# Optimization experiments

Hardware: AMD Instinct MI355X
Metric: run time of the kernel (lower is better)

## Reference

```python
import jax, jax.numpy as jnp
import numpy as np

B, S, D, H = 4, 2048, 1024, 16
DK = D // H
SCALE = float(np.sqrt(DK))
NEG_INF = jnp.float32(-1e30)


def setup_inputs() -> dict:
    key = jax.random.key(0)
    ks = jax.random.split(key, 12)
    std = 1.0 / np.sqrt(D)
    def lin(k):
        kw, kb = jax.random.split(k)
        W = jax.random.uniform(kw, (D, D), jnp.float32, -std, std)
        b = jax.random.uniform(kb, (D,), jnp.float32, -std, std)
        return W, b
    Wq, bq = lin(ks[0]); Wk, bk = lin(ks[1]); Wv, bv = lin(ks[2]); Wo, bo = lin(ks[3])
    query = jax.random.normal(ks[4], (B, S, D), jnp.float32)
    key_t = jax.random.normal(ks[5], (B, S, D), jnp.float32)
    value = jax.random.normal(ks[6], (B, S, D), jnp.float32)
    # causal mask, broadcastable to [B,H,S,S]; positions where mask==0 are blocked
    mask = jnp.tril(jnp.ones((S, S), dtype=bool))[None, None]
    return {"query": query, "key": key_t, "value": value,
            "Wq": Wq, "bq": bq, "Wk": Wk, "bk": bk, "Wv": Wv, "bv": bv,
            "Wo": Wo, "bo": bo, "mask": mask}


def reference(query, key, value, Wq, bq, Wk, bk, Wv, bv, Wo, bo, mask):
    # projections: x @ W.T + b (torch nn.Linear convention)
    q = (query @ Wq.T + bq).reshape(B, S, H, DK).transpose(0, 2, 1, 3)  # [B,H,S,DK]
    k = (key @ Wk.T + bk).reshape(B, S, H, DK).transpose(0, 2, 1, 3)
    v = (value @ Wv.T + bv).reshape(B, S, H, DK).transpose(0, 2, 1, 3)
    scores = jnp.einsum('bhqd,bhkd->bhqk', q, k) / SCALE  # [B,H,S,S]
    scores = jnp.where(mask, scores, NEG_INF)
    attn = jax.nn.softmax(scores, axis=-1)
    # dropout is identity in eval / p used at train only; omitted (p treated as 0)
    context = jnp.einsum('bhqk,bhkd->bhqd', attn, v)  # [B,H,S,DK]
    context = context.transpose(0, 2, 1, 3).reshape(B, S, D)
    return context @ Wo.T + bo
```

## Files before the change

### kernel.cpp

```cpp
#include <hip/hip_runtime.h>
#include <hip/hip_bf16.h>
#include <cstdint>
#include <cstddef>


namespace {

constexpr int B  = 4;
constexpr int S  = 2048;
constexpr int D  = 1024;
constexpr int H  = 16;
constexpr int DK = 64;
constexpr int M  = B * S;
constexpr float LOG2E    = 1.44269504088896f;
constexpr float QSCALE   = 0.125f * LOG2E;
constexpr float NEG_BIG  = -1e30f;
constexpr float DEFER_THR = 8.0f;

using bf16 = __hip_bfloat16;

typedef __attribute__((ext_vector_type(8))) __bf16 bf16x8;
typedef __attribute__((ext_vector_type(4))) float  f32x4;

__device__ __forceinline__ uint16_t f2bfu(float x) {
  uint32_t a = __builtin_bit_cast(uint32_t, x);
  return (uint16_t)((a + 0x7FFFu + ((a >> 16) & 1u)) >> 16);
}
__device__ __forceinline__ uint32_t pk2(float x, float y) {
  return (uint32_t)f2bfu(x) | ((uint32_t)f2bfu(y) << 16);
}
__device__ __forceinline__ float ex2(float x) {
  float r; asm("v_exp_f32 %0, %1" : "=v"(r) : "v"(x)); return r;
}

__device__ __forceinline__ void ldst16(const uint4* g, uint4* l) {
  __builtin_amdgcn_global_load_lds(
      (const __attribute__((address_space(1))) void*)g,
      (__attribute__((address_space(3))) void*)l, 16, 0, 0);
}

__global__ __launch_bounds__(256)
void cvt_f2b(const float* __restrict__ src, bf16* __restrict__ dst, int n8)
{
  const int i = blockIdx.x * 256 + threadIdx.x;
  if (i >= n8) return;
  const float4 a = ((const float4*)src)[2 * i];
  const float4 b = ((const float4*)src)[2 * i + 1];
  uint4 r;
  r.x = pk2(a.x, a.y); r.y = pk2(a.z, a.w);
  r.z = pk2(b.x, b.y); r.w = pk2(b.z, b.w);
  ((uint4*)dst)[i] = r;
}

template <int MODE>
__global__ __launch_bounds__(256)
void gemm128(const bf16* __restrict__ A, const bf16* __restrict__ Wb,
             const float* __restrict__ bias, void* __restrict__ out,
             int N, int K, float scale)
{
  __shared__ uint4 AsU[2][1024];
  __shared__ uint4 BsU[2][1024];

  const int tid  = threadIdx.x;
  const int w    = tid >> 6;
  const int lane = tid & 63;
  const int lm   = lane & 15;
  const int quad = lane >> 4;
  const int wm   = (w >> 1) * 64;
  const int wn   = (w & 1) * 64;

  const int row0 = blockIdx.y * 128, col0 = blockIdx.x * 128;
  const int g8 = K >> 3;

  const uint4* Ag = (const uint4*)A + (size_t)row0 * g8;
  const uint4* Bg = (const uint4*)Wb + (size_t)col0 * g8;

  f32x4 acc[4][4] = {};
  const int KT = K / 64;

#pragma unroll
  for (int i = 0; i < 4; ++i) {
    const int chunk = i * 256 + w * 64 + lane;
    const int r = chunk >> 3, c = chunk & 7;
    ldst16(&Ag[(size_t)r * g8 + c], &AsU[0][i * 256 + w * 64]);
    ldst16(&Bg[(size_t)r * g8 + c], &BsU[0][i * 256 + w * 64]);
  }

  int cur = 0;
  for (int kt = 0; kt < KT; ++kt) {
    __syncthreads();
    if (kt + 1 < KT) {
#pragma unroll
      for (int i = 0; i < 4; ++i) {
        const int chunk = i * 256 + w * 64 + lane;
        const int r = chunk >> 3, c = chunk & 7;
        ldst16(&Ag[(size_t)r * g8 + (kt + 1) * 8 + c], &AsU[cur ^ 1][i * 256 + w * 64]);
        ldst16(&Bg[(size_t)r * g8 + (kt + 1) * 8 + c], &BsU[cur ^ 1][i * 256 + w * 64]);
      }
    }
#pragma unroll
    for (int kk = 0; kk < 2; ++kk) {
      bf16x8 af[4], bfr[4];
#pragma unroll
      for (int tm = 0; tm < 4; ++tm)
        af[tm] = __builtin_bit_cast(bf16x8, AsU[cur][(wm + tm * 16 + lm) * 8 + kk * 4 + quad]);
#pragma unroll
      for (int tn = 0; tn < 4; ++tn)
        bfr[tn] = __builtin_bit_cast(bf16x8, BsU[cur][(wn + tn * 16 + lm) * 8 + kk * 4 + quad]);
#pragma unroll
      for (int tm = 0; tm < 4; ++tm)
#pragma unroll
        for (int tn = 0; tn < 4; ++tn)
          acc[tm][tn] = __builtin_amdgcn_mfma_f32_16x16x32_bf16(af[tm], bfr[tn], acc[tm][tn], 0, 0, 0);
    }
    cur ^= 1;
  }

#pragma unroll
  for (int tm = 0; tm < 4; ++tm) {
#pragma unroll
    for (int tn = 0; tn < 4; ++tn) {
      const int col = col0 + wn + tn * 16 + lm;
      const float bv = bias[col];
      if (MODE == 2) {
        float vv[4];
#pragma unroll
        for (int r = 0; r < 4; ++r) vv[r] = (acc[tm][tn][r] + bv) * scale;
        const int s0 = row0 + wm + tm * 16 + quad * 4;
        const int b_ = s0 >> 11, ss = s0 & (S - 1);
        const int h_ = col >> 6, dk = col & (DK - 1);
        uint2 st; st.x = pk2(vv[0], vv[1]); st.y = pk2(vv[2], vv[3]);
        *(uint2*)((bf16*)out + (((size_t)b_ * H + h_) * DK + dk) * S + ss) = st;
      } else {
#pragma unroll
        for (int r = 0; r < 4; ++r) {
          const int row = row0 + wm + tm * 16 + quad * 4 + r;
          const float v = (acc[tm][tn][r] + bv) * scale;
          if (MODE == 0) {
            ((float*)out)[(size_t)row * N + col] = v;
          } else {
            const int b_ = row >> 11, s_ = row & (S - 1);
            const int h_ = col >> 6,  dk = col & (DK - 1);
            ((bf16*)out)[(((size_t)b_ * H + h_) * S + s_) * DK + dk] =
                __builtin_bit_cast(bf16, f2bfu(v));
          }
        }
      }
    }
  }
}

__global__ __launch_bounds__(512)
void flash_mfma(const bf16* __restrict__ Q, const bf16* __restrict__ K,
                const bf16* __restrict__ Vt, bf16* __restrict__ ctx)
{
  __shared__ uint4 KsU[2][512];
  __shared__ uint4 VtU[2][512];
  __shared__ uint16_t PsAll[128 * 72];

  const int tid  = threadIdx.x;
  const int w    = tid >> 6;
  const int lane = tid & 63;
  const int lm   = lane & 15;
  const int quad = lane >> 4;
  const int bh   = blockIdx.x;
  const int pr   = blockIdx.y;
  const size_t base = (size_t)bh * S * DK;

  const uint4* Kg0 = (const uint4*)(K + base);
  const uint4* Vg0 = (const uint4*)(Vt + (size_t)bh * DK * S);

  const int rr   = w * 8 + (lane >> 3);
  const int csw  = (lane & 7) ^ (lane >> 3);
  const int swz0 = quad ^ (lm & 7);

  uint16_t* const Pw = PsAll + (w * 16) * 72;
  const int b_ = bh >> 4, h_ = bh & (H - 1);

  for (int pass = 0; pass < 2; ++pass) {
    const int qi = pass ? (15 - pr) : pr;
    const int q0 = qi * 128;
    const int qbase = q0 + w * 16;

    bf16x8 qf0, qf1;
    {
      const bf16* qrow = Q + base + (size_t)(qbase + lm) * DK;
      qf0 = __builtin_bit_cast(bf16x8, *(const uint4*)(qrow + quad * 8));
      qf1 = __builtin_bit_cast(bf16x8, *(const uint4*)(qrow + 32 + quad * 8));
    }

    f32x4 o[4] = {};
    float m_i[4], l_i[4];
#pragma unroll
    for (int r = 0; r < 4; ++r) { m_i[r] = NEG_BIG; l_i[r] = 0.f; }

    const int nt = 2 * qi + 2;

    ldst16(&Kg0[(size_t)rr * 8 + csw],        &KsU[0][w * 64]);
    ldst16(&Vg0[(size_t)rr * (S / 8) + csw],  &VtU[0][w * 64]);

    int cur = 0;
    for (int t = 0; t < nt; ++t) {
      __syncthreads();
      if (t + 1 < nt) {
        const int k1 = (t + 1) * 64;
        ldst16(&Kg0[(size_t)(k1 + rr) * 8 + csw],         &KsU[cur ^ 1][w * 64]);
        ldst16(&Vg0[(size_t)rr * (S / 8) + k1 / 8 + csw], &VtU[cur ^ 1][w * 64]);
      }
      const int k0 = t * 64;
      if (k0 <= qbase + 15) {
        const uint4* Ks = KsU[cur];
        const uint4* Vs = VtU[cur];

        f32x4 sc[4];
        __builtin_amdgcn_s_setprio(1);
#pragma unroll
        for (int tn = 0; tn < 4; ++tn) {
          const int row = tn * 16 + lm;
          bf16x8 kb0 = __builtin_bit_cast(bf16x8, Ks[row * 8 + swz0]);
          bf16x8 kb1 = __builtin_bit_cast(bf16x8, Ks[row * 8 + (swz0 ^ 4)]);
          sc[tn] = __builtin_amdgcn_mfma_f32_16x16x32_bf16(
                       qf0, kb0, f32x4{0.f, 0.f, 0.f, 0.f}, 0, 0, 0);
          sc[tn] = __builtin_amdgcn_mfma_f32_16x16x32_bf16(qf1, kb1, sc[tn], 0, 0, 0);
        }
        __builtin_amdgcn_s_setprio(0);

        if (k0 + 63 > qbase) {
          const int qg = qbase + quad * 4;
#pragma unroll
          for (int tn = 0; tn < 4; ++tn) {
            const int kg_ = k0 + tn * 16 + lm;
#pragma unroll
            for (int r = 0; r < 4; ++r)
              if (kg_ > qg + r) sc[tn][r] = NEG_BIG;
          }
        }

        float mr[4];
        bool need = false;
#pragma unroll
        for (int r = 0; r < 4; ++r) {
          float m4 = fmaxf(fmaxf(sc[0][r], sc[1][r]), fmaxf(sc[2][r], sc[3][r]));
#pragma unroll
          for (int off = 8; off; off >>= 1) m4 = fmaxf(m4, __shfl_xor(m4, off));
          mr[r] = m4;
          need = need || (m4 > m_i[r] + DEFER_THR);
        }
        if (__any(need)) {
#pragma unroll
          for (int r = 0; r < 4; ++r) {
            const float mn = fmaxf(m_i[r], mr[r]);
            const float al = ex2(m_i[r] - mn);
            l_i[r] *= al;
#pragma unroll
            for (int tn = 0; tn < 4; ++tn) o[tn][r] *= al;
            m_i[r] = mn;
          }
        }
#pragma unroll
        for (int r = 0; r < 4; ++r) {
          float ls = 0.f;
#pragma unroll
          for (int tn = 0; tn < 4; ++tn) {
            const float p = ex2(sc[tn][r] - m_i[r]);
            ls += p;
            Pw[(quad * 4 + r) * 72 + tn * 16 + lm] = f2bfu(p);
          }
          l_i[r] += ls;
        }

        bf16x8 ap0, ap1;
        {
          const uint16_t* prp = Pw + lm * 72 + quad * 8;
          ap0 = __builtin_bit_cast(bf16x8, *(const uint4*)prp);
          ap1 = __builtin_bit_cast(bf16x8, *(const uint4*)(prp + 32));
        }
        __builtin_amdgcn_s_setprio(1);
#pragma unroll
        for (int tn = 0; tn < 4; ++tn) {
          const int row = tn * 16 + lm;
          bf16x8 vb0 = __builtin_bit_cast(bf16x8, Vs[row * 8 + swz0]);
          bf16x8 vb1 = __builtin_bit_cast(bf16x8, Vs[row * 8 + (swz0 ^ 4)]);
          o[tn] = __builtin_amdgcn_mfma_f32_16x16x32_bf16(ap0, vb0, o[tn], 0, 0, 0);
          o[tn] = __builtin_amdgcn_mfma_f32_16x16x32_bf16(ap1, vb1, o[tn], 0, 0, 0);
        }
        __builtin_amdgcn_s_setprio(0);
      }
      cur ^= 1;
    }

    __syncthreads();
#pragma unroll
    for (int r = 0; r < 4; ++r) {
      float lr = l_i[r];
#pragma unroll
      for (int off = 8; off; off >>= 1) lr += __shfl_xor(lr, off);
      const float inv = 1.f / lr;
#pragma unroll
      for (int tn = 0; tn < 4; ++tn)
        Pw[(quad * 4 + r) * 72 + tn * 16 + lm] = f2bfu(o[tn][r] * inv);
    }
    __syncthreads();

#pragma unroll
    for (int i = 0; i < 2; ++i) {
      const int idx = tid + i * 512;
      const int row = idx >> 3, c = idx & 7;
      const uint4 v = *(const uint4*)(PsAll + row * 72 + c * 8);
      *(uint4*)(ctx + ((((size_t)b_ * S + q0 + row) * H + h_) << 6) + c * 8) = v;
    }
  }
}

}

extern "C" void kernel_launch(void* const* d_in, const int* in_sizes, int n_in,
                              void* d_out, int out_size, void* d_ws, size_t ws_size,
                              hipStream_t stream)
{
  const float* query = (const float*)d_in[0];
  const float* key_  = (const float*)d_in[1];
  const float* value = (const float*)d_in[2];
  const float* Wq    = (const float*)d_in[3];
  const float* bq    = (const float*)d_in[4];
  const float* Wk    = (const float*)d_in[5];
  const float* bk    = (const float*)d_in[6];
  const float* Wv    = (const float*)d_in[7];
  const float* bv    = (const float*)d_in[8];
  const float* Wo    = (const float*)d_in[9];
  const float* bo    = (const float*)d_in[10];

  const size_t qkv = (size_t)B * H * S * DK;
  bf16* slot0 = (bf16*)d_ws;
  bf16* slot1 = slot0 + qkv;
  bf16* slot2 = slot1 + qkv;
  bf16* slot3 = slot2 + qkv;
  bf16* inbf  = (bf16*)d_out;

  const int n8in = (int)(qkv / 8);
  const int n8w  = (D * D) / 8;
  const dim3 cvtIn(n8in / 256), cvtW(n8w / 256);
  const dim3 gproj(D / 128, M / 128);
  const dim3 gattn(B * H, 8);

  cvt_f2b<<<cvtIn, 256, 0, stream>>>(query, inbf, n8in);
  cvt_f2b<<<cvtW,  256, 0, stream>>>(Wq, slot3, n8w);
  gemm128<1><<<gproj, 256, 0, stream>>>(inbf, slot3, bq, slot0, D, D, QSCALE);
  cvt_f2b<<<cvtIn, 256, 0, stream>>>(key_, inbf, n8in);
  cvt_f2b<<<cvtW,  256, 0, stream>>>(Wk, slot3, n8w);
  gemm128<1><<<gproj, 256, 0, stream>>>(inbf, slot3, bk, slot1, D, D, 1.0f);
  cvt_f2b<<<cvtIn, 256, 0, stream>>>(value, inbf, n8in);
  cvt_f2b<<<cvtW,  256, 0, stream>>>(Wv, slot3, n8w);
  gemm128<2><<<gproj, 256, 0, stream>>>(inbf, slot3, bv, slot2, D, D, 1.0f);
  flash_mfma<<<gattn, 512, 0, stream>>>(slot0, slot1, slot2, slot3);
  cvt_f2b<<<cvtW, 256, 0, stream>>>(Wo, slot0, n8w);
  gemm128<0><<<gproj, 256, 0, stream>>>(slot3, slot0, bo, d_out, D, D, 1.0f);
}
```

Baseline: 384.1 us.

## Keep softmax P in registers via transposed QK MFMA and batch conversions

```diff
diff --git a/kernel.cpp b/kernel.cpp
--- a/kernel.cpp
+++ b/kernel.cpp
@@ -12,9 +12,9 @@
 constexpr int H  = 16;
 constexpr int DK = 64;
 constexpr int M  = B * S;
-constexpr float LOG2E    = 1.44269504088896f;
-constexpr float QSCALE   = 0.125f * LOG2E;
-constexpr float NEG_BIG  = -1e30f;
+constexpr float LOG2E     = 1.44269504088896f;
+constexpr float QSCALE    = 0.125f * LOG2E;
+constexpr float NEG_BIG   = -1e30f;
 constexpr float DEFER_THR = 8.0f;
 
 using bf16 = __hip_bfloat16;
@@ -31,6 +31,14 @@
 }
 __device__ __forceinline__ float ex2(float x) {
   float r; asm("v_exp_f32 %0, %1" : "=v"(r) : "v"(x)); return r;
+}
+__device__ __forceinline__ uint32_t cvtpk(float lo, float hi) {
+  uint32_t r;
+  asm("v_cvt_pk_bf16_f32 %0, %1, %2" : "=v"(r) : "v"(lo), "v"(hi));
+  return r;
+}
+__device__ __forceinline__ float hmax4(f32x4 v) {
+  return fmaxf(fmaxf(v[0], v[1]), fmaxf(v[2], v[3]));
 }
 
 __device__ __forceinline__ void ldst16(const uint4* g, uint4* l) {
@@ -40,15 +48,20 @@
 }
 
 __global__ __launch_bounds__(256)
-void cvt_f2b(const float* __restrict__ src, bf16* __restrict__ dst, int n8)
+void cvt3(const float* __restrict__ a, const float* __restrict__ b,
+          const float* __restrict__ c, bf16* __restrict__ x,
+          bf16* __restrict__ y, bf16* __restrict__ z_, int n8)
 {
+  const int zz = blockIdx.y;
+  const float* src = (zz == 0) ? a : (zz == 1) ? b : c;
+  bf16*        dst = (zz == 0) ? x : (zz == 1) ? y : z_;
   const int i = blockIdx.x * 256 + threadIdx.x;
   if (i >= n8) return;
-  const float4 a = ((const float4*)src)[2 * i];
-  const float4 b = ((const float4*)src)[2 * i + 1];
+  const float4 p = ((const float4*)src)[2 * i];
+  const float4 q = ((const float4*)src)[2 * i + 1];
   uint4 r;
-  r.x = pk2(a.x, a.y); r.y = pk2(a.z, a.w);
-  r.z = pk2(b.x, b.y); r.w = pk2(b.z, b.w);
+  r.x = pk2(p.x, p.y); r.y = pk2(p.z, p.w);
+  r.z = pk2(q.x, q.y); r.w = pk2(q.z, q.w);
   ((uint4*)dst)[i] = r;
 }
 
@@ -156,7 +169,7 @@
 {
   __shared__ uint4 KsU[2][512];
   __shared__ uint4 VtU[2][512];
-  __shared__ uint16_t PsAll[128 * 72];
+  __shared__ uint16_t Os[128 * 72];
 
   const int tid  = threadIdx.x;
   const int w    = tid >> 6;
@@ -170,11 +183,12 @@
   const uint4* Kg0 = (const uint4*)(K + base);
   const uint4* Vg0 = (const uint4*)(Vt + (size_t)bh * DK * S);
 
-  const int rr   = w * 8 + (lane >> 3);
-  const int csw  = (lane & 7) ^ (lane >> 3);
-  const int swz0 = quad ^ (lm & 7);
-
-  uint16_t* const Pw = PsAll + (w * 16) * 72;
+  const int rr  = w * 8 + (lane >> 3);
+  const int csw = (lane & 7) ^ (lane >> 3) ^ ((w & 1) << 2);
+  const int fv  = (lm & 7) ^ (((lm >> 3) & 1) << 2);
+  const int r0  = ((lm >> 2) << 3) | (lm & 3);
+
+  uint16_t* const Ow = Os + (w * 16) * 72;
   const int b_ = bh >> 4, h_ = bh & (H - 1);
 
   for (int pass = 0; pass < 2; ++pass) {
@@ -190,14 +204,12 @@
     }
 
     f32x4 o[4] = {};
-    float m_i[4], l_i[4];
-#pragma unroll
-    for (int r = 0; r < 4; ++r) { m_i[r] = NEG_BIG; l_i[r] = 0.f; }
+    float m_i = NEG_BIG, l_i = 0.f;
 
     const int nt = 2 * qi + 2;
 
-    ldst16(&Kg0[(size_t)rr * 8 + csw],        &KsU[0][w * 64]);
-    ldst16(&Vg0[(size_t)rr * (S / 8) + csw],  &VtU[0][w * 64]);
+    ldst16(&Kg0[(size_t)rr * 8 + csw],       &KsU[0][w * 64]);
+    ldst16(&Vg0[(size_t)rr * (S / 8) + csw], &VtU[0][w * 64]);
 
     int cur = 0;
     for (int t = 0; t < nt; ++t) {
@@ -216,71 +228,71 @@
         __builtin_amdgcn_s_setprio(1);
 #pragma unroll
         for (int tn = 0; tn < 4; ++tn) {
-          const int row = tn * 16 + lm;
-          bf16x8 kb0 = __builtin_bit_cast(bf16x8, Ks[row * 8 + swz0]);
-          bf16x8 kb1 = __builtin_bit_cast(bf16x8, Ks[row * 8 + (swz0 ^ 4)]);
+          const int row = r0 + ((tn & 1) << 2) + ((tn >> 1) << 5);
+          const int fr  = (row & 7) ^ (((row >> 3) & 1) << 2);
+          const int cb  = quad ^ fr;
+          bf16x8 kb0 = __builtin_bit_cast(bf16x8, Ks[row * 8 + cb]);
+          bf16x8 kb1 = __builtin_bit_cast(bf16x8, Ks[row * 8 + (cb ^ 4)]);
           sc[tn] = __builtin_amdgcn_mfma_f32_16x16x32_bf16(
-                       qf0, kb0, f32x4{0.f, 0.f, 0.f, 0.f}, 0, 0, 0);
-          sc[tn] = __builtin_amdgcn_mfma_f32_16x16x32_bf16(qf1, kb1, sc[tn], 0, 0, 0);
+                       kb0, qf0, f32x4{0.f, 0.f, 0.f, 0.f}, 0, 0, 0);
+          sc[tn] = __builtin_amdgcn_mfma_f32_16x16x32_bf16(kb1, qf1, sc[tn], 0, 0, 0);
         }
         __builtin_amdgcn_s_setprio(0);
 
         if (k0 + 63 > qbase) {
-          const int qg = qbase + quad * 4;
+          const int qg = qbase + lm;
 #pragma unroll
           for (int tn = 0; tn < 4; ++tn) {
-            const int kg_ = k0 + tn * 16 + lm;
+            const int kb_ = k0 + ((tn >> 1) << 5) + (quad << 3) + ((tn & 1) << 2);
 #pragma unroll
             for (int r = 0; r < 4; ++r)
-              if (kg_ > qg + r) sc[tn][r] = NEG_BIG;
+              if (kb_ + r > qg) sc[tn][r] = NEG_BIG;
           }
         }
 
-        float mr[4];
-        bool need = false;
-#pragma unroll
-        for (int r = 0; r < 4; ++r) {
-          float m4 = fmaxf(fmaxf(sc[0][r], sc[1][r]), fmaxf(sc[2][r], sc[3][r]));
-#pragma unroll
-          for (int off = 8; off; off >>= 1) m4 = fmaxf(m4, __shfl_xor(m4, off));
-          mr[r] = m4;
-          need = need || (m4 > m_i[r] + DEFER_THR);
-        }
-        if (__any(need)) {
-#pragma unroll
-          for (int r = 0; r < 4; ++r) {
-            const float mn = fmaxf(m_i[r], mr[r]);
-            const float al = ex2(m_i[r] - mn);
-            l_i[r] *= al;
-#pragma unroll
-            for (int tn = 0; tn < 4; ++tn) o[tn][r] *= al;
-            m_i[r] = mn;
+        float mloc = fmaxf(fmaxf(hmax4(sc[0]), hmax4(sc[1])),
+                           fmaxf(hmax4(sc[2]), hmax4(sc[3])));
+        mloc = fmaxf(mloc, __shfl_xor(mloc, 16));
+        mloc = fmaxf(mloc, __shfl_xor(mloc, 32));
+
+        if (__any(mloc > m_i + DEFER_THR)) {
+          const float mn = fmaxf(m_i, mloc);
+          const float al = ex2(m_i - mn);
+          l_i *= al; m_i = mn;
+          const float a0 = __shfl(al, quad * 4 + 0, 16);
+          const float a1 = __shfl(al, quad * 4 + 1, 16);
+          const float a2 = __shfl(al, quad * 4 + 2, 16);
+          const float a3 = __shfl(al, quad * 4 + 3, 16);
+#pragma unroll
+          for (int tn = 0; tn < 4; ++tn) {
+            o[tn][0] *= a0; o[tn][1] *= a1; o[tn][2] *= a2; o[tn][3] *= a3;
           }
         }
-#pragma unroll
-        for (int r = 0; r < 4; ++r) {
-          float ls = 0.f;
-#pragma unroll
-          for (int tn = 0; tn < 4; ++tn) {
-            const float p = ex2(sc[tn][r] - m_i[r]);
-            ls += p;
-            Pw[(quad * 4 + r) * 72 + tn * 16 + lm] = f2bfu(p);
-          }
-          l_i[r] += ls;
-        }
-
-        bf16x8 ap0, ap1;
-        {
-          const uint16_t* prp = Pw + lm * 72 + quad * 8;
-          ap0 = __builtin_bit_cast(bf16x8, *(const uint4*)prp);
-          ap1 = __builtin_bit_cast(bf16x8, *(const uint4*)(prp + 32));
-        }
+
+        float ls = 0.f;
+#pragma unroll
+        for (int tn = 0; tn < 4; ++tn) {
+#pragma unroll
+          for (int r = 0; r < 4; ++r) sc[tn][r] = ex2(sc[tn][r] - m_i);
+          ls += (sc[tn][0] + sc[tn][1]) + (sc[tn][2] + sc[tn][3]);
+        }
+        l_i += ls;
+
+        uint4 pw0, pw1;
+        pw0.x = cvtpk(sc[0][0], sc[0][1]); pw0.y = cvtpk(sc[0][2], sc[0][3]);
+        pw0.z = cvtpk(sc[1][0], sc[1][1]); pw0.w = cvtpk(sc[1][2], sc[1][3]);
+        pw1.x = cvtpk(sc[2][0], sc[2][1]); pw1.y = cvtpk(sc[2][2], sc[2][3]);
+        pw1.z = cvtpk(sc[3][0], sc[3][1]); pw1.w = cvtpk(sc[3][2], sc[3][3]);
+        const bf16x8 ap0 = __builtin_bit_cast(bf16x8, pw0);
+        const bf16x8 ap1 = __builtin_bit_cast(bf16x8, pw1);
+
         __builtin_amdgcn_s_setprio(1);
 #pragma unroll
         for (int tn = 0; tn < 4; ++tn) {
-          const int row = tn * 16 + lm;
-          bf16x8 vb0 = __builtin_bit_cast(bf16x8, Vs[row * 8 + swz0]);
-          bf16x8 vb1 = __builtin_bit_cast(bf16x8, Vs[row * 8 + (swz0 ^ 4)]);
+          const int vrow = tn * 16 + lm;
+          const int cv = quad ^ fv;
+          bf16x8 vb0 = __builtin_bit_cast(bf16x8, Vs[vrow * 8 + cv]);
+          bf16x8 vb1 = __builtin_bit_cast(bf16x8, Vs[vrow * 8 + (cv ^ 4)]);
           o[tn] = __builtin_amdgcn_mfma_f32_16x16x32_bf16(ap0, vb0, o[tn], 0, 0, 0);
           o[tn] = __builtin_amdgcn_mfma_f32_16x16x32_bf16(ap1, vb1, o[tn], 0, 0, 0);
         }
@@ -290,15 +302,22 @@
     }
 
     __syncthreads();
-#pragma unroll
-    for (int r = 0; r < 4; ++r) {
-      float lr = l_i[r];
-#pragma unroll
-      for (int off = 8; off; off >>= 1) lr += __shfl_xor(lr, off);
+    {
+      float lr = l_i;
+      lr += __shfl_xor(lr, 16);
+      lr += __shfl_xor(lr, 32);
       const float inv = 1.f / lr;
-#pragma unroll
-      for (int tn = 0; tn < 4; ++tn)
-        Pw[(quad * 4 + r) * 72 + tn * 16 + lm] = f2bfu(o[tn][r] * inv);
+      const float i0 = __shfl(inv, quad * 4 + 0, 16);
+      const float i1 = __shfl(inv, quad * 4 + 1, 16);
+      const float i2 = __shfl(inv, quad * 4 + 2, 16);
+      const float i3 = __shfl(inv, quad * 4 + 3, 16);
+#pragma unroll
+      for (int tn = 0; tn < 4; ++tn) {
+        Ow[(quad * 4 + 0) * 72 + tn * 16 + lm] = f2bfu(o[tn][0] * i0);
+        Ow[(quad * 4 + 1) * 72 + tn * 16 + lm] = f2bfu(o[tn][1] * i1);
+        Ow[(quad * 4 + 2) * 72 + tn * 16 + lm] = f2bfu(o[tn][2] * i2);
+        Ow[(quad * 4 + 3) * 72 + tn * 16 + lm] = f2bfu(o[tn][3] * i3);
+      }
     }
     __syncthreads();
 
@@ -306,7 +325,7 @@
     for (int i = 0; i < 2; ++i) {
       const int idx = tid + i * 512;
       const int row = idx >> 3, c = idx & 7;
-      const uint4 v = *(const uint4*)(PsAll + row * 72 + c * 8);
+      const uint4 v = *(const uint4*)(Os + row * 72 + c * 8);
       *(uint4*)(ctx + ((((size_t)b_ * S + q0 + row) * H + h_) << 6) + c * 8) = v;
     }
   }
@@ -331,28 +350,30 @@
   const float* bo    = (const float*)d_in[10];
 
   const size_t qkv = (size_t)B * H * S * DK;
+  const size_t DD  = (size_t)D * D;
   bf16* slot0 = (bf16*)d_ws;
   bf16* slot1 = slot0 + qkv;
   bf16* slot2 = slot1 + qkv;
   bf16* slot3 = slot2 + qkv;
-  bf16* inbf  = (bf16*)d_out;
+  bf16* dout0 = (bf16*)d_out;
+  bf16* dout1 = dout0 + qkv;
 
   const int n8in = (int)(qkv / 8);
-  const int n8w  = (D * D) / 8;
-  const dim3 cvtIn(n8in / 256), cvtW(n8w / 256);
+  const int n8w  = (int)(DD / 8);
   const dim3 gproj(D / 128, M / 128);
   const dim3 gattn(B * H, 8);
 
-  cvt_f2b<<<cvtIn, 256, 0, stream>>>(query, inbf, n8in);
-  cvt_f2b<<<cvtW,  256, 0, stream>>>(Wq, slot3, n8w);
-  gemm128<1><<<gproj, 256, 0, stream>>>(inbf, slot3, bq, slot0, D, D, QSCALE);
-  cvt_f2b<<<cvtIn, 256, 0, stream>>>(key_, inbf, n8in);
-  cvt_f2b<<<cvtW,  256, 0, stream>>>(Wk, slot3, n8w);
-  gemm128<1><<<gproj, 256, 0, stream>>>(inbf, slot3, bk, slot1, D, D, 1.0f);
-  cvt_f2b<<<cvtIn, 256, 0, stream>>>(value, inbf, n8in);
-  cvt_f2b<<<cvtW,  256, 0, stream>>>(Wv, slot3, n8w);
-  gemm128<2><<<gproj, 256, 0, stream>>>(inbf, slot3, bv, slot2, D, D, 1.0f);
+  cvt3<<<dim3(n8in / 256, 3), 256, 0, stream>>>(query, key_, value,
+                                                dout0, dout1, slot3, n8in);
+  cvt3<<<dim3(n8w / 256, 2), 256, 0, stream>>>(Wq, Wk, Wk,
+                                               slot2, slot2 + DD, slot2, n8w);
+  gemm128<1><<<gproj, 256, 0, stream>>>(dout0, slot2, bq, slot0, D, D, QSCALE);
+  gemm128<1><<<gproj, 256, 0, stream>>>(dout1, slot2 + DD, bk, slot1, D, D, 1.0f);
+  cvt3<<<dim3(n8w / 256, 1), 256, 0, stream>>>(Wv, Wv, Wv,
+                                               dout0, dout0, dout0, n8w);
+  gemm128<2><<<gproj, 256, 0, stream>>>(slot3, dout0, bv, slot2, D, D, 1.0f);
   flash_mfma<<<gattn, 512, 0, stream>>>(slot0, slot1, slot2, slot3);
-  cvt_f2b<<<cvtW, 256, 0, stream>>>(Wo, slot0, n8w);
+  cvt3<<<dim3(n8w / 256, 1), 256, 0, stream>>>(Wo, Wo, Wo,
+                                               slot0, slot0, slot0, n8w);
   gemm128<0><<<gproj, 256, 0, stream>>>(slot3, slot0, bo, d_out, D, D, 1.0f);
 }
```

After: 343.4 us. 10.6% less time.
